# Performance work log

Measured on AMD Instinct MI355X. Metric: run time of the kernel, lower is better.

The kernel has to match this reference:

```python
import jax, jax.numpy as jnp
import numpy as np

TAU = 0.07
EPS_LOG = 1e-6
EPS_DEN = 1e-8
EPS_NORM = 1e-12


def setup_inputs() -> dict:
    key = jax.random.key(0)
    k1, k2, k3, k4 = jax.random.split(key, 4)
    B, C, H, W = 24, 4, 256, 256
    D = 64
    pred = jax.random.uniform(k1, (B, C, H, W), dtype=jnp.float32)
    proj = jax.random.normal(k2, (3, B, D, H, W), dtype=jnp.float32)
    mask = jax.random.randint(k3, (B, H, W), 0, 2).astype(jnp.int32)
    pseudo_label = jax.random.randint(k4, (B, H, W), 0, 4).astype(jnp.int32)
    return {"pred": pred, "proj": proj, "mask": mask,
            "pseudo_label": pseudo_label, "idx": 0, "sample_num": 5}


def reference(pred, proj, mask, pseudo_label, idx, sample_num):
    B = mask.shape[0]
    D = proj.shape[2]
    # uncertainty: sum over channel dim -> (B, H*W)
    unc = jnp.sum(pred * jnp.log(pred + EPS_LOG), axis=1).reshape(B, -1)
    # (3,B,D,H,W) -> (3,B,HW,D), L2-normalize along feature dim
    p = proj.transpose(0, 1, 3, 4, 2).reshape(proj.shape[0], B, -1, D)
    p = p / jnp.maximum(jnp.linalg.norm(p, axis=-1, keepdims=True), EPS_NORM)
    curr = p[idx]                                               # (B,HW,D)
    pos = jnp.stack([p[i] for i in range(p.shape[0]) if i != idx], axis=1)  # (B,P,HW,D)
    # top-k most 'certain' pixels per batch element
    _, top_idx = jax.lax.top_k(unc, sample_num)                 # (B,S)
    c_sel = jnp.take_along_axis(curr, top_idx[:, :, None], axis=1)          # (B,S,D)
    p_sel = jnp.take_along_axis(pos, top_idx[:, None, :, None], axis=2)     # (B,P,S,D)
    # vectors are unit-norm, so cosine similarity == dot product
    pos_sim = jnp.einsum('bsd,bpsd->bs', c_sel, p_sel)          # sum over positives
    pos_loss = jnp.exp(pos_sim / TAU)                           # (B,S)
    mat = jnp.exp(jnp.einsum('bid,bjd->bij', c_sel, c_sel) / TAU)  # (B,S,S)
    neg_loss = mat.sum(axis=1) - jnp.diagonal(mat, axis1=1, axis2=2)  # (B,S)
    per_b = -jnp.log(pos_loss / (pos_loss + neg_loss + EPS_DEN)).mean(axis=1)
    return per_b.sum() / B
```

## Files before the change

### kernel.cpp

```cpp
#include <hip/hip_runtime.h>
#include <float.h>
#include <limits.h>
#include <math.h>

constexpr int kB = 24;
constexpr int kC = 4;
constexpr int kHW = 65536;
constexpr int kD = 64;
constexpr int kNChunk = 32;
constexpr int kChunk = kHW / kNChunk;
constexpr int kMaxS = 8;
constexpr float kTau = 0.07f;
constexpr float kEpsLog = 1e-6f;
constexpr float kEpsDen = 1e-8f;
constexpr float kEpsNorm = 1e-12f;

__device__ __forceinline__ unsigned long long packKey(float v, unsigned int pix) {
    unsigned int x = __float_as_uint(v);
    unsigned int m = (x & 0x80000000u) ? ~x : (x | 0x80000000u);
    return ((unsigned long long)m << 32) | (unsigned long long)(~pix);
}

__device__ __forceinline__ unsigned long long u64max(unsigned long long a, unsigned long long b) {
    return a > b ? a : b;
}

__device__ __forceinline__ unsigned long long shfl_xor_u64(unsigned long long k, int m) {
    int lo = __shfl_xor((int)(unsigned int)k, m, 64);
    int hi = __shfl_xor((int)(unsigned int)(k >> 32), m, 64);
    return ((unsigned long long)(unsigned int)hi << 32) | (unsigned long long)(unsigned int)lo;
}

__device__ __forceinline__ unsigned long long waveMax64(unsigned long long k) {
    #pragma unroll
    for (int o = 32; o > 0; o >>= 1) k = u64max(k, shfl_xor_u64(k, o));
    return k;
}

__device__ __forceinline__ float wave_sum(float x) {
    #pragma unroll
    for (int o = 32; o > 0; o >>= 1) x += __shfl_xor(x, o, 64);
    return x;
}

__global__ __launch_bounds__(256) void k_topk(
        const float* __restrict__ pred,
        unsigned long long* __restrict__ cand) {
    const int t = threadIdx.x;
    const int lane = t & 63;
    const int wave = t >> 6;
    const int b = blockIdx.x / kNChunk;
    const int chunk = blockIdx.x % kNChunk;
    const int j0 = chunk * kChunk + t * 8;
    const float* pb = pred + (size_t)b * kC * kHW + j0;

    float u[8];
    #pragma unroll
    for (int i = 0; i < 8; ++i) u[i] = 0.f;
    #pragma unroll
    for (int c = 0; c < kC; ++c) {
        float4 a = *reinterpret_cast<const float4*>(pb + (size_t)c * kHW);
        float4 d = *reinterpret_cast<const float4*>(pb + (size_t)c * kHW + 4);
        u[0] += a.x * __logf(a.x + kEpsLog);
        u[1] += a.y * __logf(a.y + kEpsLog);
        u[2] += a.z * __logf(a.z + kEpsLog);
        u[3] += a.w * __logf(a.w + kEpsLog);
        u[4] += d.x * __logf(d.x + kEpsLog);
        u[5] += d.y * __logf(d.y + kEpsLog);
        u[6] += d.z * __logf(d.z + kEpsLog);
        u[7] += d.w * __logf(d.w + kEpsLog);
    }
    unsigned long long key[8];
    #pragma unroll
    for (int i = 0; i < 8; ++i) key[i] = packKey(u[i], (unsigned int)(j0 + i));

    __shared__ unsigned long long waveCand[4][kMaxS];
    #pragma unroll
    for (int r = 0; r < kMaxS; ++r) {
        unsigned long long my = key[0];
        #pragma unroll
        for (int i = 1; i < 8; ++i) my = u64max(my, key[i]);
        unsigned long long w = waveMax64(my);
        if (lane == 0) waveCand[wave][r] = w;
        #pragma unroll
        for (int i = 0; i < 8; ++i) if (key[i] == w) key[i] = 0ull;
    }
    __syncthreads();
    if (t >= 64) return;

    unsigned long long mine = (lane < 4 * kMaxS) ? waveCand[lane >> 3][lane & 7] : 0ull;
    unsigned long long* myCand = cand + (size_t)blockIdx.x * kMaxS;
    #pragma unroll
    for (int r = 0; r < kMaxS; ++r) {
        unsigned long long w = waveMax64(mine);
        if (lane == 0) myCand[r] = w;
        if (mine == w) mine = 0ull;
    }
}

__global__ __launch_bounds__(64) void k_loss(
        const float* __restrict__ proj, const int* __restrict__ idxp,
        const int* __restrict__ snum, const unsigned long long* __restrict__ cand,
        float* __restrict__ per_b) {
    int S = snum[0];
    S = S < 1 ? 1 : (S > kMaxS ? kMaxS : S);
    const int b = blockIdx.x;
    const int lane = threadIdx.x;

    const unsigned long long* bc = cand + (size_t)b * kNChunk * kMaxS;
    unsigned long long c0 = bc[lane], c1 = bc[lane + 64],
                       c2 = bc[lane + 128], c3 = bc[lane + 192];
    int topPix[kMaxS];
    #pragma unroll
    for (int r = 0; r < kMaxS; ++r) {
        unsigned long long m2 = u64max(u64max(c0, c1), u64max(c2, c3));
        unsigned long long w = waveMax64(m2);
        topPix[r] = (int)(~(unsigned int)w);
        if (c0 == w) c0 = 0ull;
        if (c1 == w) c1 = 0ull;
        if (c2 == w) c2 = 0ull;
        if (c3 == w) c3 = 0ull;
    }

    int idx0 = idxp[0];
    idx0 = idx0 < 0 ? 0 : (idx0 > 2 ? 2 : idx0);
    const int v1 = (idx0 == 0) ? 1 : 0;
    const int v2 = (idx0 == 2) ? 1 : 2;

    float cc[kMaxS], x1[kMaxS], x2[kMaxS];
    #pragma unroll
    for (int s = 0; s < kMaxS; ++s) {
        cc[s] = 0.f; x1[s] = 0.f; x2[s] = 0.f;
        if (s < S) {
            const size_t off = (size_t)lane * kHW + (size_t)(unsigned int)topPix[s];
            cc[s] = proj[((size_t)(idx0 * kB + b) * kD) * kHW + off];
            x1[s] = proj[((size_t)(v1  * kB + b) * kD) * kHW + off];
            x2[s] = proj[((size_t)(v2  * kB + b) * kD) * kHW + off];
        }
    }
    float cv[kMaxS], ap[kMaxS];
    #pragma unroll
    for (int s = 0; s < kMaxS; ++s) {
        cv[s] = 0.f; ap[s] = 0.f;
        if (s < S) {
            const float c  = cc[s] / fmaxf(sqrtf(wave_sum(cc[s] * cc[s])), kEpsNorm);
            const float a1 = x1[s] / fmaxf(sqrtf(wave_sum(x1[s] * x1[s])), kEpsNorm);
            const float a2 = x2[s] / fmaxf(sqrtf(wave_sum(x2[s] * x2[s])), kEpsNorm);
            cv[s] = c; ap[s] = a1 + a2;
        }
    }
    float pl[kMaxS];
    #pragma unroll
    for (int s = 0; s < kMaxS; ++s) {
        pl[s] = 0.f;
        if (s < S) pl[s] = expf(wave_sum(cv[s] * ap[s]) / kTau);
    }
    float neg[kMaxS];
    #pragma unroll
    for (int s = 0; s < kMaxS; ++s) neg[s] = 0.f;
    #pragma unroll
    for (int i = 0; i < kMaxS; ++i) {
        if (i < S) {
            #pragma unroll
            for (int j = i + 1; j < kMaxS; ++j) {
                if (j < S) {
                    const float e = expf(wave_sum(cv[i] * cv[j]) / kTau);
                    neg[i] += e; neg[j] += e;
                }
            }
        }
    }
    float acc = 0.f;
    #pragma unroll
    for (int s = 0; s < kMaxS; ++s)
        if (s < S) acc += -logf(pl[s] / (pl[s] + neg[s] + kEpsDen));
    if (lane == 0) per_b[b] = acc / (float)S;
}

__global__ void k_finalize(const float* __restrict__ per_b, float* __restrict__ out) {
    if (threadIdx.x == 0 && blockIdx.x == 0) {
        float s = 0.f;
        for (int b = 0; b < kB; ++b) s += per_b[b];
        out[0] = s / (float)kB;
    }
}

extern "C" void kernel_launch(void* const* d_in, const int* in_sizes, int n_in,
                              void* d_out, int out_size, void* d_ws, size_t ws_size,
                              hipStream_t stream) {
    const float* pred = (const float*)d_in[0];
    const float* proj = (const float*)d_in[1];
    const int* idxp  = (const int*)d_in[4];
    const int* snump = (const int*)d_in[5];
    float* out = (float*)d_out;

    char* ws = (char*)d_ws;
    unsigned long long* cand = (unsigned long long*)ws;
    float* per_b = (float*)(ws + (size_t)kB * kNChunk * kMaxS * 8);

    k_topk<<<kB * kNChunk, 256, 0, stream>>>(pred, cand);
    k_loss<<<kB, 64, 0, stream>>>(proj, idxp, snump, cand, per_b);
    k_finalize<<<1, 64, 0, stream>>>(per_b, out);
}
```

Before: 29.08 us.

## Fuse loss and finalize into one block and drop in-block candidate merge

```diff
diff --git a/kernel.cpp b/kernel.cpp
--- a/kernel.cpp
+++ b/kernel.cpp
@@ -9,7 +9,9 @@
 constexpr int kD = 64;
 constexpr int kNChunk = 32;
 constexpr int kChunk = kHW / kNChunk;
+constexpr int kWaves = 4;
 constexpr int kMaxS = 8;
+constexpr int kSlotsPerBatch = kNChunk * kWaves * kMaxS;
 constexpr float kTau = 0.07f;
 constexpr float kEpsLog = 1e-6f;
 constexpr float kEpsDen = 1e-8f;
@@ -17,7 +19,7 @@
 
 __device__ __forceinline__ unsigned long long packKey(float v, unsigned int pix) {
     unsigned int x = __float_as_uint(v);
-    unsigned int m = (x & 0x80000000u) ? ~x : (x | 0x80000000u);
+    unsigned int m = x ^ (((unsigned int)((int)x >> 31)) | 0x80000000u);
     return ((unsigned long long)m << 32) | (unsigned long long)(~pix);
 }
 
@@ -44,8 +46,10 @@
 }
 
 __global__ __launch_bounds__(256) void k_topk(
-        const float* __restrict__ pred,
+        const float* __restrict__ pred, const int* __restrict__ snum,
         unsigned long long* __restrict__ cand) {
+    int S = snum[0];
+    S = S < 1 ? 1 : (S > kMaxS ? kMaxS : S);
     const int t = threadIdx.x;
     const int lane = t & 63;
     const int wave = t >> 6;
@@ -74,113 +78,112 @@
     #pragma unroll
     for (int i = 0; i < 8; ++i) key[i] = packKey(u[i], (unsigned int)(j0 + i));
 
-    __shared__ unsigned long long waveCand[4][kMaxS];
-    #pragma unroll
-    for (int r = 0; r < kMaxS; ++r) {
+    unsigned long long* myCand = cand + ((size_t)blockIdx.x * kWaves + wave) * kMaxS;
+    for (int r = 0; r < S; ++r) {
         unsigned long long my = key[0];
         #pragma unroll
         for (int i = 1; i < 8; ++i) my = u64max(my, key[i]);
-        unsigned long long w = waveMax64(my);
-        if (lane == 0) waveCand[wave][r] = w;
+        const unsigned long long w = waveMax64(my);
+        if (lane == 0) myCand[r] = w;
         #pragma unroll
         for (int i = 0; i < 8; ++i) if (key[i] == w) key[i] = 0ull;
     }
-    __syncthreads();
-    if (t >= 64) return;
-
-    unsigned long long mine = (lane < 4 * kMaxS) ? waveCand[lane >> 3][lane & 7] : 0ull;
-    unsigned long long* myCand = cand + (size_t)blockIdx.x * kMaxS;
-    #pragma unroll
-    for (int r = 0; r < kMaxS; ++r) {
-        unsigned long long w = waveMax64(mine);
-        if (lane == 0) myCand[r] = w;
-        if (mine == w) mine = 0ull;
-    }
-}
-
-__global__ __launch_bounds__(64) void k_loss(
+}
+
+__global__ __launch_bounds__(1024) void k_loss_final(
         const float* __restrict__ proj, const int* __restrict__ idxp,
         const int* __restrict__ snum, const unsigned long long* __restrict__ cand,
-        float* __restrict__ per_b) {
+        float* __restrict__ out) {
     int S = snum[0];
     S = S < 1 ? 1 : (S > kMaxS ? kMaxS : S);
-    const int b = blockIdx.x;
-    const int lane = threadIdx.x;
-
-    const unsigned long long* bc = cand + (size_t)b * kNChunk * kMaxS;
-    unsigned long long c0 = bc[lane], c1 = bc[lane + 64],
-                       c2 = bc[lane + 128], c3 = bc[lane + 192];
-    int topPix[kMaxS];
-    #pragma unroll
-    for (int r = 0; r < kMaxS; ++r) {
-        unsigned long long m2 = u64max(u64max(c0, c1), u64max(c2, c3));
-        unsigned long long w = waveMax64(m2);
-        topPix[r] = (int)(~(unsigned int)w);
-        if (c0 == w) c0 = 0ull;
-        if (c1 == w) c1 = 0ull;
-        if (c2 == w) c2 = 0ull;
-        if (c3 == w) c3 = 0ull;
-    }
+    const int lane = threadIdx.x & 63;
+    const int wave = threadIdx.x >> 6;
+
+    __shared__ float per_b[kB];
 
     int idx0 = idxp[0];
     idx0 = idx0 < 0 ? 0 : (idx0 > 2 ? 2 : idx0);
     const int v1 = (idx0 == 0) ? 1 : 0;
     const int v2 = (idx0 == 2) ? 1 : 2;
 
-    float cc[kMaxS], x1[kMaxS], x2[kMaxS];
-    #pragma unroll
-    for (int s = 0; s < kMaxS; ++s) {
-        cc[s] = 0.f; x1[s] = 0.f; x2[s] = 0.f;
-        if (s < S) {
-            const size_t off = (size_t)lane * kHW + (size_t)(unsigned int)topPix[s];
-            cc[s] = proj[((size_t)(idx0 * kB + b) * kD) * kHW + off];
-            x1[s] = proj[((size_t)(v1  * kB + b) * kD) * kHW + off];
-            x2[s] = proj[((size_t)(v2  * kB + b) * kD) * kHW + off];
-        }
-    }
-    float cv[kMaxS], ap[kMaxS];
-    #pragma unroll
-    for (int s = 0; s < kMaxS; ++s) {
-        cv[s] = 0.f; ap[s] = 0.f;
-        if (s < S) {
-            const float c  = cc[s] / fmaxf(sqrtf(wave_sum(cc[s] * cc[s])), kEpsNorm);
-            const float a1 = x1[s] / fmaxf(sqrtf(wave_sum(x1[s] * x1[s])), kEpsNorm);
-            const float a2 = x2[s] / fmaxf(sqrtf(wave_sum(x2[s] * x2[s])), kEpsNorm);
-            cv[s] = c; ap[s] = a1 + a2;
-        }
-    }
-    float pl[kMaxS];
-    #pragma unroll
-    for (int s = 0; s < kMaxS; ++s) {
-        pl[s] = 0.f;
-        if (s < S) pl[s] = expf(wave_sum(cv[s] * ap[s]) / kTau);
-    }
-    float neg[kMaxS];
-    #pragma unroll
-    for (int s = 0; s < kMaxS; ++s) neg[s] = 0.f;
-    #pragma unroll
-    for (int i = 0; i < kMaxS; ++i) {
-        if (i < S) {
-            #pragma unroll
-            for (int j = i + 1; j < kMaxS; ++j) {
-                if (j < S) {
-                    const float e = expf(wave_sum(cv[i] * cv[j]) / kTau);
-                    neg[i] += e; neg[j] += e;
+    for (int b = wave; b < kB; b += 16) {
+        const unsigned long long* bc = cand + (size_t)b * kSlotsPerBatch;
+        unsigned long long c[16];
+        #pragma unroll
+        for (int k = 0; k < 16; ++k) {
+            const int sid = lane + 64 * k;
+            const unsigned long long v = bc[sid];
+            c[k] = ((sid & (kMaxS - 1)) < S) ? v : 0ull;
+        }
+        int topPix[kMaxS];
+        #pragma unroll
+        for (int r = 0; r < kMaxS; ++r) {
+            topPix[r] = 0;
+            if (r < S) {
+                unsigned long long my = c[0];
+                #pragma unroll
+                for (int k = 1; k < 16; ++k) my = u64max(my, c[k]);
+                const unsigned long long w = waveMax64(my);
+                topPix[r] = (int)(~(unsigned int)w);
+                #pragma unroll
+                for (int k = 0; k < 16; ++k) if (c[k] == w) c[k] = 0ull;
+            }
+        }
+
+        float cc[kMaxS], x1[kMaxS], x2[kMaxS];
+        #pragma unroll
+        for (int s = 0; s < kMaxS; ++s) {
+            cc[s] = 0.f; x1[s] = 0.f; x2[s] = 0.f;
+            if (s < S) {
+                const size_t off = (size_t)lane * kHW + (size_t)(unsigned int)topPix[s];
+                cc[s] = proj[((size_t)(idx0 * kB + b) * kD) * kHW + off];
+                x1[s] = proj[((size_t)(v1  * kB + b) * kD) * kHW + off];
+                x2[s] = proj[((size_t)(v2  * kB + b) * kD) * kHW + off];
+            }
+        }
+        float cv[kMaxS], ap[kMaxS];
+        #pragma unroll
+        for (int s = 0; s < kMaxS; ++s) {
+            cv[s] = 0.f; ap[s] = 0.f;
+            if (s < S) {
+                const float c0 = cc[s] / fmaxf(sqrtf(wave_sum(cc[s] * cc[s])), kEpsNorm);
+                const float a1 = x1[s] / fmaxf(sqrtf(wave_sum(x1[s] * x1[s])), kEpsNorm);
+                const float a2 = x2[s] / fmaxf(sqrtf(wave_sum(x2[s] * x2[s])), kEpsNorm);
+                cv[s] = c0; ap[s] = a1 + a2;
+            }
+        }
+        float pl[kMaxS];
+        #pragma unroll
+        for (int s = 0; s < kMaxS; ++s) {
+            pl[s] = 0.f;
+            if (s < S) pl[s] = expf(wave_sum(cv[s] * ap[s]) / kTau);
+        }
+        float neg[kMaxS];
+        #pragma unroll
+        for (int s = 0; s < kMaxS; ++s) neg[s] = 0.f;
+        #pragma unroll
+        for (int i = 0; i < kMaxS; ++i) {
+            if (i < S) {
+                #pragma unroll
+                for (int j = i + 1; j < kMaxS; ++j) {
+                    if (j < S) {
+                        const float e = expf(wave_sum(cv[i] * cv[j]) / kTau);
+                        neg[i] += e; neg[j] += e;
+                    }
                 }
             }
         }
-    }
-    float acc = 0.f;
-    #pragma unroll
-    for (int s = 0; s < kMaxS; ++s)
-        if (s < S) acc += -logf(pl[s] / (pl[s] + neg[s] + kEpsDen));
-    if (lane == 0) per_b[b] = acc / (float)S;
-}
-
-__global__ void k_finalize(const float* __restrict__ per_b, float* __restrict__ out) {
-    if (threadIdx.x == 0 && blockIdx.x == 0) {
+        float acc = 0.f;
+        #pragma unroll
+        for (int s = 0; s < kMaxS; ++s)
+            if (s < S) acc += -logf(pl[s] / (pl[s] + neg[s] + kEpsDen));
+        if (lane == 0) per_b[b] = acc / (float)S;
+    }
+
+    __syncthreads();
+    if (threadIdx.x == 0) {
         float s = 0.f;
-        for (int b = 0; b < kB; ++b) s += per_b[b];
+        for (int i = 0; i < kB; ++i) s += per_b[i];
         out[0] = s / (float)kB;
     }
 }
@@ -194,11 +197,8 @@
     const int* snump = (const int*)d_in[5];
     float* out = (float*)d_out;
 
-    char* ws = (char*)d_ws;
-    unsigned long long* cand = (unsigned long long*)ws;
-    float* per_b = (float*)(ws + (size_t)kB * kNChunk * kMaxS * 8);
-
-    k_topk<<<kB * kNChunk, 256, 0, stream>>>(pred, cand);
-    k_loss<<<kB, 64, 0, stream>>>(proj, idxp, snump, cand, per_b);
-    k_finalize<<<1, 64, 0, stream>>>(per_b, out);
-}
+    unsigned long long* cand = (unsigned long long*)d_ws;
+
+    k_topk<<<kB * kNChunk, 256, 0, stream>>>(pred, snump, cand);
+    k_loss_final<<<1, 1024, 0, stream>>>(proj, idxp, snump, cand, out);
+}
```

Measured after the change: 53.81 us. 85.0% more time.
